# Optimization experiments

Measured on AMD Instinct MI355X. Metric: run time of the kernel, lower is better.

## Reference

```python
import jax, jax.numpy as jnp
import numpy as np

N_GRAPHS = 64
NODES_PER_G = 640
N = N_GRAPHS * NODES_PER_G      # 40960 nodes
DEG = 16
E = N * DEG                     # 655360 edges
D = 128                         # hidden_dim == out_dim
POS = 16                        # pos_enc_dim
L = 4                           # n GatedGCN-LSPE layers
N_ATOM = 28
N_BOND = 4
EPS = 1e-6
BN_EPS = 1e-5


def _lin(x, w, b):
    return x @ w + b


def _bn(x, g, b):
    # torch BatchNorm1d training forward: biased batch stats
    m = x.mean(0)
    v = x.var(0)
    return (x - m) * jax.lax.rsqrt(v + BN_EPS) * g + b


def setup_inputs() -> dict:
    key = jax.random.key(0)
    ks = iter(jax.random.split(key, 64))
    def nrm(shape, s=0.1):
        return jax.random.normal(next(ks), shape, dtype=jnp.float32) * s
    h_atoms = jax.random.randint(next(ks), (N,), 0, N_ATOM)
    e_bonds = jax.random.randint(next(ks), (E,), 0, N_BOND)
    # keep edges within each graph of the batch
    epg = E // N_GRAPHS
    off = (jnp.arange(E) // epg) * NODES_PER_G
    src = jax.random.randint(next(ks), (E,), 0, NODES_PER_G) + off
    dst = jax.random.randint(next(ks), (E,), 0, NODES_PER_G) + off
    node_graph_ids = jnp.arange(N) // NODES_PER_G
    return dict(
        h_atoms=h_atoms, e_bonds=e_bonds, src=src, dst=dst,
        node_graph_ids=node_graph_ids,
        p=nrm((N, POS), 1.0),
        W_emb_h=nrm((N_ATOM, D)), W_emb_p=nrm((POS, D)), b_emb_p=nrm((D,)),
        W_emb_e=nrm((N_BOND, D)),
        A1_w=nrm((L, 2 * D, D)), A1_b=nrm((L, D)),
        A2_w=nrm((L, 2 * D, D)), A2_b=nrm((L, D)),
        B1_w=nrm((L, D, D)), B1_b=nrm((L, D)),
        B2_w=nrm((L, D, D)), B2_b=nrm((L, D)),
        B3_w=nrm((L, D, D)), B3_b=nrm((L, D)),
        C1_w=nrm((L, D, D)), C1_b=nrm((L, D)),
        C2_w=nrm((L, D, D)), C2_b=nrm((L, D)),
        bn_h_g=jnp.ones((L, D)), bn_h_b=jnp.zeros((L, D)),
        bn_e_g=jnp.ones((L, D)), bn_e_b=jnp.zeros((L, D)),
        p_out_w=nrm((D, POS)), p_out_b=nrm((POS,)),
        Whp_w=nrm((D + POS, D)), Whp_b=nrm((D,)),
        mlp_w0=nrm((D, D // 2)), mlp_b0=nrm((D // 2,)),
        mlp_w1=nrm((D // 2, D // 4)), mlp_b1=nrm((D // 4,)),
        mlp_w2=nrm((D // 4, 1)), mlp_b2=nrm((1,)),
    )


def _forward(p, W_emb_h, W_emb_p, b_emb_p, W_emb_e,
             A1_w, A1_b, A2_w, A2_b, B1_w, B1_b, B2_w, B2_b, B3_w, B3_b,
             C1_w, C1_b, C2_w, C2_b, bn_h_g, bn_h_b, bn_e_g, bn_e_b,
             p_out_w, p_out_b, Whp_w, Whp_b,
             mlp_w0, mlp_b0, mlp_w1, mlp_b1, mlp_w2, mlp_b2,
             h_atoms, e_bonds, src, dst, node_graph_ids):
    seg = lambda x, idx, n: jax.ops.segment_sum(x, idx, num_segments=n)
    h = W_emb_h[h_atoms]                      # [N,D] atom embedding
    pc = _lin(p, W_emb_p, b_emb_p)            # [N,D] PE embedding
    ef = W_emb_e[e_bonds]                     # [E,D] bond embedding
    for l in range(L):
        h_in, p_in, e_in = h, pc, ef
        # edge gates: hat_eta_ij = B1 h_i + B2 h_j + B3 e_ij (u=src, v=dst)
        hat_eta = (_lin(h, B1_w[l], B1_b[l])[src]
                   + _lin(h, B2_w[l], B2_b[l])[dst]
                   + _lin(ef, B3_w[l], B3_b[l]))          # [E,D]
        sig = jax.nn.sigmoid(hat_eta)
        eta = sig / (seg(sig, dst, N)[dst] + EPS)          # normalized gate
        hp = jnp.concatenate([h, pc], axis=-1)             # [N,2D]
        h_new = _lin(hp, A1_w[l], A1_b[l]) + seg(eta * _lin(hp, A2_w[l], A2_b[l])[src], dst, N)
        p_new = _lin(pc, C1_w[l], C1_b[l]) + seg(eta * _lin(pc, C2_w[l], C2_b[l])[src], dst, N)
        h_new = jax.nn.relu(_bn(h_new, bn_h_g[l], bn_h_b[l]))
        e_new = jax.nn.relu(_bn(hat_eta, bn_e_g[l], bn_e_b[l]))
        p_new = jnp.tanh(p_new)
        h = h_in + h_new       # residual (in_dim==out_dim)
        pc = p_in + p_new
        ef = e_in + e_new
    # pe_init == 'rand_walk' post-processing
    po = _lin(pc, p_out_w, p_out_b)                        # [N,POS]
    po = po - (seg(po, node_graph_ids, N_GRAPHS) / NODES_PER_G)[node_graph_ids]
    po = po / jnp.sqrt(seg(po * po, node_graph_ids, N_GRAPHS))[node_graph_ids]
    hp2 = _lin(jnp.concatenate([h, po], axis=-1), Whp_w, Whp_b)
    hg = seg(hp2, node_graph_ids, N_GRAPHS) / NODES_PER_G  # mean readout [G,D]
    y = jax.nn.relu(_lin(hg, mlp_w0, mlp_b0))
    y = jax.nn.relu(_lin(y, mlp_w1, mlp_b1))
    return _lin(y, mlp_w2, mlp_b2)                         # [G,1]


def reference(h_atoms, e_bonds, src, dst, node_graph_ids, p,
              W_emb_h, W_emb_p, b_emb_p, W_emb_e,
              A1_w, A1_b, A2_w, A2_b, B1_w, B1_b, B2_w, B2_b, B3_w, B3_b,
              C1_w, C1_b, C2_w, C2_b, bn_h_g, bn_h_b, bn_e_g, bn_e_b,
              p_out_w, p_out_b, Whp_w, Whp_b,
              mlp_w0, mlp_b0, mlp_w1, mlp_b1, mlp_w2, mlp_b2):
    return _forward(p, W_emb_h, W_emb_p, b_emb_p, W_emb_e,
                    A1_w, A1_b, A2_w, A2_b, B1_w, B1_b, B2_w, B2_b, B3_w, B3_b,
                    C1_w, C1_b, C2_w, C2_b, bn_h_g, bn_h_b, bn_e_g, bn_e_b,
                    p_out_w, p_out_b, Whp_w, Whp_b,
                    mlp_w0, mlp_b0, mlp_w1, mlp_b1, mlp_w2, mlp_b2,
                    h_atoms, e_bonds, src, dst, node_graph_ids)
```

## Files before the change

kernel.cpp:

```cpp
#include <hip/hip_runtime.h>
#include <math.h>

#define N_NODES 40960
#define N_EDGES 655360
#define NPG     640
#define NGRAPH  64
#define DH      128
#define NLAYERS 4
#define GATE_EPS 1e-6f
#define BN_EPS   1e-5f

#define POOL_BYTES 560000000ull
__device__ __attribute__((aligned(256))) unsigned char g_pool[POOL_BYTES];

using short8  = __attribute__((ext_vector_type(8))) short;
using float4v = __attribute__((ext_vector_type(4))) float;

static __device__ __forceinline__ float sigmoidf_(float x) {
  return 1.f / (1.f + __expf(-x));
}
static __device__ __forceinline__ unsigned short f2bf(float f) {
  unsigned int u = __float_as_uint(f);
  unsigned int r = 0x7FFFu + ((u >> 16) & 1u);
  return (unsigned short)((u + r) >> 16);
}
static __device__ __forceinline__ float bf2f(unsigned short h) {
  return __uint_as_float(((unsigned int)h) << 16);
}

template <int WITH_STATS>
__global__ __launch_bounds__(256)
void egemm(const unsigned short* __restrict__ ef,
           const unsigned short* __restrict__ Wt,
           const float* __restrict__ bias,
           unsigned short* __restrict__ hat,
           const int* __restrict__ srcp, const int* __restrict__ dstp,
           const float* __restrict__ G1, const float* __restrict__ G2,
           float* __restrict__ stats)
{
  __shared__ __align__(16) unsigned char smem[128 * 136 * 2];
  auto Ws   = reinterpret_cast<unsigned short (*)[136]>(smem);
  auto hatL = reinterpret_cast<float (*)[132]>(smem);

  const int t    = threadIdx.x;
  const int w    = t >> 6;
  const int lane = t & 63;
  const int quad = lane >> 4;
  const int l16  = lane & 15;
  const size_t row0 = (size_t)blockIdx.x * 64;

  const size_t arow = row0 + w * 16 + l16;
  short8 a[4];
#pragma unroll
  for (int ks = 0; ks < 4; ++ks)
    a[ks] = *reinterpret_cast<const short8*>(&ef[arow * 128 + ks * 32 + quad * 8]);

#pragma unroll
  for (int i = 0; i < 8; ++i) {
    int flat = i * 256 + t;
    int n = flat >> 4, g = flat & 15;
    *reinterpret_cast<uint4*>(&Ws[n][g * 8]) =
        *reinterpret_cast<const uint4*>(&Wt[n * 128 + g * 8]);
  }
  __syncthreads();

  float4v acc[8];
#pragma unroll
  for (int j = 0; j < 8; ++j) acc[j] = (float4v){0.f, 0.f, 0.f, 0.f};

#pragma unroll
  for (int ks = 0; ks < 4; ++ks) {
#pragma unroll
    for (int j = 0; j < 8; ++j) {
      short8 b = *reinterpret_cast<const short8*>(&Ws[j * 16 + l16][ks * 32 + quad * 8]);
      acc[j] = __builtin_amdgcn_mfma_f32_16x16x32_bf16(a[ks], b, acc[j], 0, 0, 0);
    }
  }

  __syncthreads();
#pragma unroll
  for (int j = 0; j < 8; ++j)
#pragma unroll
    for (int r = 0; r < 4; ++r)
      hatL[w * 16 + quad * 4 + r][j * 16 + l16] = acc[j][r];
  __syncthreads();

  {
    const int r   = t >> 2;
    const int c0  = (t & 3) * 32;
    const size_t row = row0 + r;
    const int si = srcp[row], di = dstp[row];
    const float* g1p = &G1[(size_t)si * 128 + c0];
    const float* g2p = &G2[(size_t)di * 128 + c0];
    const float* bp  = &bias[c0];
#pragma unroll
    for (int q2 = 0; q2 < 4; ++q2) {
      float4 h0 = *reinterpret_cast<const float4*>(&hatL[r][c0 + q2 * 8]);
      float4 h1 = *reinterpret_cast<const float4*>(&hatL[r][c0 + q2 * 8 + 4]);
      float4 b0 = *reinterpret_cast<const float4*>(&bp[q2 * 8]);
      float4 b1 = *reinterpret_cast<const float4*>(&bp[q2 * 8 + 4]);
      float4 x0 = *reinterpret_cast<const float4*>(&g1p[q2 * 8]);
      float4 x1 = *reinterpret_cast<const float4*>(&g1p[q2 * 8 + 4]);
      float4 y0 = *reinterpret_cast<const float4*>(&g2p[q2 * 8]);
      float4 y1 = *reinterpret_cast<const float4*>(&g2p[q2 * 8 + 4]);
      float v[8] = {h0.x + b0.x + x0.x + y0.x, h0.y + b0.y + x0.y + y0.y,
                    h0.z + b0.z + x0.z + y0.z, h0.w + b0.w + x0.w + y0.w,
                    h1.x + b1.x + x1.x + y1.x, h1.y + b1.y + x1.y + y1.y,
                    h1.z + b1.z + x1.z + y1.z, h1.w + b1.w + x1.w + y1.w};
      unsigned int pk[4];
      float vr[8];
#pragma unroll
      for (int i = 0; i < 4; ++i) {
        unsigned short lo = f2bf(v[2 * i]), hi = f2bf(v[2 * i + 1]);
        pk[i] = (unsigned int)lo | ((unsigned int)hi << 16);
        vr[2 * i] = bf2f(lo); vr[2 * i + 1] = bf2f(hi);
      }
      uint4 st; st.x = pk[0]; st.y = pk[1]; st.z = pk[2]; st.w = pk[3];
      *reinterpret_cast<uint4*>(&hat[row * 128 + c0 + q2 * 8]) = st;
      if (WITH_STATS) {
        float4 w0; w0.x = vr[0]; w0.y = vr[1]; w0.z = vr[2]; w0.w = vr[3];
        float4 w1; w1.x = vr[4]; w1.y = vr[5]; w1.z = vr[6]; w1.w = vr[7];
        *reinterpret_cast<float4*>(&hatL[r][c0 + q2 * 8]) = w0;
        *reinterpret_cast<float4*>(&hatL[r][c0 + q2 * 8 + 4]) = w1;
      }
    }
  }

  if constexpr (WITH_STATS) {
    __syncthreads();
    if (t < 128) {
      float s = 0.f, q = 0.f;
#pragma unroll 8
      for (int r = 0; r < 64; ++r) {
        float v = hatL[r][t];
        s += v; q += v * v;
      }
      atomicAdd(&stats[t], s);
      atomicAdd(&stats[128 + t], q);
    }
  }
}

__global__ __launch_bounds__(256)
void ngemm6(const unsigned short* __restrict__ hp,
            const unsigned short* __restrict__ WtL,
            const float* __restrict__ B1b, const float* __restrict__ B2b,
            const float* __restrict__ A1b, const float* __restrict__ A2b,
            const float* __restrict__ C1b, const float* __restrict__ C2b,
            float* __restrict__ B1h, float* __restrict__ B2h,
            float* __restrict__ A1hp, float* __restrict__ A2hp,
            float* __restrict__ C1p, float* __restrict__ C2p)
{
  __shared__ unsigned short As[64][264];

  const int t    = threadIdx.x;
  const int w    = t >> 6;
  const int lane = t & 63;
  const int quad = lane >> 4;
  const int l16  = lane & 15;
  const size_t row0 = (size_t)blockIdx.x * 64;

#pragma unroll
  for (int i = 0; i < 8; ++i) {
    int flat = i * 256 + t;
    int r = flat >> 5, g = flat & 31;
    *reinterpret_cast<uint4*>(&As[r][g * 8]) =
        *reinterpret_cast<const uint4*>(&hp[(row0 + r) * 256 + g * 8]);
  }
  __syncthreads();

  const unsigned short* Wm[6] = {WtL, WtL + 16384, WtL + 49152, WtL + 81920,
                                 WtL + 114688, WtL + 131072};
  const int Kk[6]   = {128, 128, 256, 256, 128, 128};
  const int koff[6] = {0, 0, 0, 0, 128, 128};
  const float* bs[6] = {B1b, B2b, A1b, A2b, C1b, C2b};
  float* outp[6] = {B1h, B2h, A1hp, A2hp, C1p, C2p};

  for (int m = 0; m < 6; ++m) {
    const unsigned short* W = Wm[m];
    const int K = Kk[m], ko = koff[m];
    float4v acc[8];
#pragma unroll
    for (int j = 0; j < 8; ++j) acc[j] = (float4v){0.f, 0.f, 0.f, 0.f};
    for (int ks = 0; ks < K / 32; ++ks) {
      short8 a = *reinterpret_cast<const short8*>(&As[w * 16 + l16][ko + ks * 32 + quad * 8]);
#pragma unroll
      for (int j = 0; j < 8; ++j) {
        short8 b = *reinterpret_cast<const short8*>(&W[(size_t)(j * 16 + l16) * K + ks * 32 + quad * 8]);
        acc[j] = __builtin_amdgcn_mfma_f32_16x16x32_bf16(a, b, acc[j], 0, 0, 0);
      }
    }
    float* o = outp[m];
    const float* bb = bs[m];
#pragma unroll
    for (int j = 0; j < 8; ++j) {
      int col = j * 16 + l16;
      float bc = bb[col];
#pragma unroll
      for (int r = 0; r < 4; ++r) {
        size_t orow = row0 + w * 16 + quad * 4 + r;
        o[orow * 128 + col] = acc[j][r] + bc;
      }
    }
  }
}

__global__ void prep_weights(const float* __restrict__ B1, const float* __restrict__ B2,
                             const float* __restrict__ B3, const float* __restrict__ A1,
                             const float* __restrict__ A2, const float* __restrict__ C1,
                             const float* __restrict__ C2, unsigned short* __restrict__ Wt)
{
  int idx = blockIdx.x * 256 + threadIdx.x;
  if (idx >= 4 * 147456) return;
  int layer = idx / 147456;
  int o = idx - layer * 147456;
  const float* src; int K, local;
  if (o < 16384)       { src = B1 + layer * 16384; local = o;          K = 128; }
  else if (o < 32768)  { src = B2 + layer * 16384; local = o - 16384;  K = 128; }
  else if (o < 49152)  { src = B3 + layer * 16384; local = o - 32768;  K = 128; }
  else if (o < 81920)  { src = A1 + layer * 32768; local = o - 49152;  K = 256; }
  else if (o < 114688) { src = A2 + layer * 32768; local = o - 81920;  K = 256; }
  else if (o < 131072) { src = C1 + layer * 16384; local = o - 114688; K = 128; }
  else                 { src = C2 + layer * 16384; local = o - 131072; K = 128; }
  int n = local / K, k = local - n * K;
  Wt[idx] = f2bf(src[k * 128 + n]);
}

__global__ void convert_hp(const float* __restrict__ h, const float* __restrict__ pc,
                           unsigned short* __restrict__ hp)
{
  int t = blockIdx.x * 256 + threadIdx.x;
  if (t >= N_NODES * 64) return;
  int n = t >> 6, part = t & 63;
  float4 v = (part < 32) ? reinterpret_cast<const float4*>(h)[n * 32 + part]
                         : reinterpret_cast<const float4*>(pc)[n * 32 + (part - 32)];
  ushort4 o;
  o.x = f2bf(v.x); o.y = f2bf(v.y); o.z = f2bf(v.z); o.w = f2bf(v.w);
  reinterpret_cast<ushort4*>(hp)[n * 64 + part] = o;
}

__global__ void embed_nodes_k(const int* __restrict__ idx, const float* __restrict__ table,
                              float* __restrict__ out, int M)
{
  int t = blockIdx.x * 256 + threadIdx.x;
  if (t < M * 32) {
    int r = t >> 5, c = t & 31;
    reinterpret_cast<float4*>(out)[t] =
        reinterpret_cast<const float4*>(table)[idx[r] * 32 + c];
  }
}

__global__ void embed_edges_bf(const int* __restrict__ bonds, const int* __restrict__ eidx,
                               const float* __restrict__ table,
                               unsigned short* __restrict__ out, int M)
{
  int t = blockIdx.x * 256 + threadIdx.x;
  if (t < M * 32) {
    int r = t >> 5, c = t & 31;
    float4 v = reinterpret_cast<const float4*>(table)[bonds[eidx[r]] * 32 + c];
    ushort4 o;
    o.x = f2bf(v.x); o.y = f2bf(v.y); o.z = f2bf(v.z); o.w = f2bf(v.w);
    reinterpret_cast<ushort4*>(out)[t] = o;
  }
}

__global__ void hist_k(const int* __restrict__ dstI, int* __restrict__ deg, int E)
{
  int e = blockIdx.x * 256 + threadIdx.x;
  if (e < E) atomicAdd(&deg[dstI[e]], 1);
}

__global__ void scan_k(const int* __restrict__ deg, int* __restrict__ row_start,
                       int* __restrict__ cursor, int n)
{
  __shared__ int buf[1024];
  __shared__ int carry;
  int t = threadIdx.x;
  if (t == 0) carry = 0;
  __syncthreads();
  for (int b0 = 0; b0 < n; b0 += 1024) {
    int v = (b0 + t < n) ? deg[b0 + t] : 0;
    buf[t] = v;
    __syncthreads();
    for (int off = 1; off < 1024; off <<= 1) {
      int add = (t >= off) ? buf[t - off] : 0;
      __syncthreads();
      buf[t] += add;
      __syncthreads();
    }
    int incl = buf[t];
    int excl = carry + incl - v;
    if (b0 + t < n) { row_start[b0 + t] = excl; cursor[b0 + t] = excl; }
    __syncthreads();
    if (t == 1023) carry += incl;
    __syncthreads();
  }
  if (t == 0) row_start[n] = carry;
}

__global__ void fill_k(const int* __restrict__ dstI, int* __restrict__ cursor,
                       int* __restrict__ eidx, int E)
{
  int e = blockIdx.x * 256 + threadIdx.x;
  if (e < E) {
    int p = atomicAdd(&cursor[dstI[e]], 1);
    eidx[p] = e;
  }
}

__global__ void permute_sd(const int* __restrict__ eidx, const int* __restrict__ srcI,
                           const int* __restrict__ dstI, int* __restrict__ srcp,
                           int* __restrict__ dstp, int E)
{
  int e = blockIdx.x * 256 + threadIdx.x;
  if (e < E) {
    int o = eidx[e];
    srcp[e] = srcI[o];
    dstp[e] = dstI[o];
  }
}

template <int EF_UPD>
__global__ __launch_bounds__(256)
void gate_agg4(const unsigned short* __restrict__ hat, const int* __restrict__ row_start,
               const int* __restrict__ srcp,
               const float* __restrict__ A1hp, const float* __restrict__ A2hp,
               const float* __restrict__ C1p, const float* __restrict__ C2p,
               float* __restrict__ hraw, float* __restrict__ pc,
               unsigned short* __restrict__ ef, const float* __restrict__ ss_e,
               unsigned short* __restrict__ hp)
{
  int t = threadIdx.x;
  int node = blockIdx.x * 4 + (t >> 6);
  int lane = t & 63;
  int c = lane * 2;
  int beg = row_start[node], end = row_start[node + 1];

  float s0 = 0.f, s1 = 0.f;
  for (int e = beg; e < end; ++e) {
    ushort2 hv = *reinterpret_cast<const ushort2*>(&hat[(size_t)e * 128 + c]);
    s0 += sigmoidf_(bf2f(hv.x));
    s1 += sigmoidf_(bf2f(hv.y));
  }
  float inv0 = 1.f / (s0 + GATE_EPS);
  float inv1 = 1.f / (s1 + GATE_EPS);

  float2 eA, eB;
  if (EF_UPD) {
    eA = *reinterpret_cast<const float2*>(&ss_e[c]);
    eB = *reinterpret_cast<const float2*>(&ss_e[128 + c]);
  }

  float ha0 = 0.f, ha1 = 0.f, pa0 = 0.f, pa1 = 0.f;
  for (int e = beg; e < end; ++e) {
    int s = srcp[e];
    ushort2 hv = *reinterpret_cast<const ushort2*>(&hat[(size_t)e * 128 + c]);
    float hx = bf2f(hv.x), hy = bf2f(hv.y);
    float w0 = sigmoidf_(hx) * inv0;
    float w1 = sigmoidf_(hy) * inv1;
    float2 a2 = *reinterpret_cast<const float2*>(&A2hp[(size_t)s * 128 + c]);
    float2 c2 = *reinterpret_cast<const float2*>(&C2p[(size_t)s * 128 + c]);
    ha0 += w0 * a2.x; ha1 += w1 * a2.y;
    pa0 += w0 * c2.x; pa1 += w1 * c2.y;
    if (EF_UPD) {
      ushort2 ev = *reinterpret_cast<ushort2*>(&ef[(size_t)e * 128 + c]);
      float ex = bf2f(ev.x) + fmaxf(hx * eA.x + eB.x, 0.f);
      float ey = bf2f(ev.y) + fmaxf(hy * eA.y + eB.y, 0.f);
      ushort2 eo; eo.x = f2bf(ex); eo.y = f2bf(ey);
      *reinterpret_cast<ushort2*>(&ef[(size_t)e * 128 + c]) = eo;
    }
  }
  size_t ix = (size_t)node * 128 + c;
  float2 a1 = *reinterpret_cast<const float2*>(&A1hp[ix]);
  float2 c1 = *reinterpret_cast<const float2*>(&C1p[ix]);
  float2 hv; hv.x = a1.x + ha0; hv.y = a1.y + ha1;
  *reinterpret_cast<float2*>(&hraw[ix]) = hv;
  float2 pv = *reinterpret_cast<float2*>(&pc[ix]);
  pv.x += tanhf(c1.x + pa0);
  pv.y += tanhf(c1.y + pa1);
  *reinterpret_cast<float2*>(&pc[ix]) = pv;
  ushort2 ph; ph.x = f2bf(pv.x); ph.y = f2bf(pv.y);
  *reinterpret_cast<ushort2*>(&hp[(size_t)node * 256 + 128 + c]) = ph;
}

__global__ __launch_bounds__(128)
void col_stats(const float* __restrict__ x, float* __restrict__ stats, int rowsPerBlock)
{
  int d = threadIdx.x;
  size_t r0 = (size_t)blockIdx.x * rowsPerBlock;
  float s = 0.f, q = 0.f;
  for (int i = 0; i < rowsPerBlock; ++i) {
    float v = x[(r0 + i) * 128 + d];
    s += v; q += v * v;
  }
  atomicAdd(&stats[d], s);
  atomicAdd(&stats[128 + d], q);
}

__global__ void bn_finalize(const float* __restrict__ stats, const float* __restrict__ g,
                            const float* __restrict__ b, float invM, float* __restrict__ ss)
{
  int c = threadIdx.x;
  float m = stats[c] * invM;
  float v = stats[128 + c] * invM - m * m;
  float A = rsqrtf(v + BN_EPS) * g[c];
  ss[c] = A;
  ss[128 + c] = b[c] - m * A;
}

__global__ void apply_h(float* __restrict__ dest, const float* __restrict__ xraw,
                        const float* __restrict__ ss, unsigned short* __restrict__ hp,
                        int total4)
{
  int t = blockIdx.x * 256 + threadIdx.x;
  if (t >= total4) return;
  int c4 = t & 31, n = t >> 5;
  float4 x = reinterpret_cast<const float4*>(xraw)[t];
  float4 A = reinterpret_cast<const float4*>(ss)[c4];
  float4 B = reinterpret_cast<const float4*>(ss + 128)[c4];
  float4 dv = reinterpret_cast<float4*>(dest)[t];
  dv.x += fmaxf(x.x * A.x + B.x, 0.f);
  dv.y += fmaxf(x.y * A.y + B.y, 0.f);
  dv.z += fmaxf(x.z * A.z + B.z, 0.f);
  dv.w += fmaxf(x.w * A.w + B.w, 0.f);
  reinterpret_cast<float4*>(dest)[t] = dv;
  ushort4 o;
  o.x = f2bf(dv.x); o.y = f2bf(dv.y); o.z = f2bf(dv.z); o.w = f2bf(dv.w);
  *reinterpret_cast<ushort4*>(&hp[(size_t)n * 256 + c4 * 4]) = o;
}

template <int MODE>
__global__ __launch_bounds__(256)
void gemm_k(const float* __restrict__ Xa, int Ka,
            const float* __restrict__ Xb, int Kb,
            const float* __restrict__ W,
            const float* __restrict__ bias,
            float* __restrict__ out,
            float* __restrict__ hg, float inv_nodes, int npg)
{
  __shared__ float Xs[16][68];
  __shared__ float Ws[16][128];
  __shared__ float red[8][128];

  const int t  = threadIdx.x;
  const int ty = t >> 5;
  const int tx = t & 31;
  const int row0 = blockIdx.x * 64;
  const int K = Ka + Kb;

  float acc[8][4];
#pragma unroll
  for (int i = 0; i < 8; ++i)
#pragma unroll
    for (int j = 0; j < 4; ++j) acc[i][j] = 0.f;

  const int xr = t >> 2;
  const int xk = (t & 3) << 2;
  const int wr = t >> 5;
  const int wc = tx << 2;

  for (int kk = 0; kk < K; kk += 16) {
    const float* xbase; int ldk, kloc;
    if (kk < Ka) { xbase = Xa; ldk = Ka; kloc = kk; }
    else         { xbase = Xb; ldk = Kb; kloc = kk - Ka; }
    float4 xv = *reinterpret_cast<const float4*>(
        &xbase[(size_t)(row0 + xr) * ldk + kloc + xk]);
    Xs[xk + 0][xr] = xv.x; Xs[xk + 1][xr] = xv.y;
    Xs[xk + 2][xr] = xv.z; Xs[xk + 3][xr] = xv.w;

    float4 wv0 = *reinterpret_cast<const float4*>(&W[(size_t)(kk + wr) * 128 + wc]);
    float4 wv1 = *reinterpret_cast<const float4*>(&W[(size_t)(kk + wr + 8) * 128 + wc]);
    *reinterpret_cast<float4*>(&Ws[wr][wc])     = wv0;
    *reinterpret_cast<float4*>(&Ws[wr + 8][wc]) = wv1;
    __syncthreads();

#pragma unroll
    for (int k = 0; k < 16; ++k) {
      float4 b4 = *reinterpret_cast<const float4*>(&Ws[k][wc]);
      float4 a0 = *reinterpret_cast<const float4*>(&Xs[k][ty << 3]);
      float4 a1 = *reinterpret_cast<const float4*>(&Xs[k][(ty << 3) + 4]);
      float a[8] = {a0.x, a0.y, a0.z, a0.w, a1.x, a1.y, a1.z, a1.w};
      float b[4] = {b4.x, b4.y, b4.z, b4.w};
#pragma unroll
      for (int i = 0; i < 8; ++i) {
        acc[i][0] += a[i] * b[0];
        acc[i][1] += a[i] * b[1];
        acc[i][2] += a[i] * b[2];
        acc[i][3] += a[i] * b[3];
      }
    }
    __syncthreads();
  }

  float4 bb = *reinterpret_cast<const float4*>(&bias[wc]);
  float bv[4] = {bb.x, bb.y, bb.z, bb.w};

  if (MODE == 0) {
#pragma unroll
    for (int i = 0; i < 8; ++i) {
      int r = row0 + (ty << 3) + i;
      float4 ov;
      ov.x = acc[i][0] + bv[0]; ov.y = acc[i][1] + bv[1];
      ov.z = acc[i][2] + bv[2]; ov.w = acc[i][3] + bv[3];
      *reinterpret_cast<float4*>(&out[(size_t)r * 128 + wc]) = ov;
    }
  } else {
    float csum[4] = {0, 0, 0, 0};
#pragma unroll
    for (int i = 0; i < 8; ++i) {
      csum[0] += acc[i][0]; csum[1] += acc[i][1];
      csum[2] += acc[i][2]; csum[3] += acc[i][3];
    }
#pragma unroll
    for (int j = 0; j < 4; ++j) red[ty][wc + j] = csum[j];
    __syncthreads();
    if (ty == 0) {
      int g = row0 / npg;
#pragma unroll
      for (int j = 0; j < 4; ++j) {
        float s = 0;
#pragma unroll
        for (int q = 0; q < 8; ++q) s += red[q][wc + j];
        atomicAdd(&hg[(size_t)g * 128 + wc + j], (s + 64.f * bv[j]) * inv_nodes);
      }
    }
  }
}

__global__ __launch_bounds__(256)
void po_gemm(const float* __restrict__ pc, const float* __restrict__ w,
             const float* __restrict__ b, float* __restrict__ po)
{
  __shared__ float pcs[16][128];
  __shared__ float wl[128][16];
  int t = threadIdx.x;
  int n0 = blockIdx.x * 16;
  for (int i = t; i < 512; i += 256) {
    int r = i >> 5, c = (i & 31) << 2;
    *reinterpret_cast<float4*>(&pcs[r][c]) =
        *reinterpret_cast<const float4*>(&pc[(size_t)(n0 + r) * 128 + c]);
  }
  for (int i = t; i < 512; i += 256) {
    int r = i >> 2, c = (i & 3) << 2;
    *reinterpret_cast<float4*>(&wl[r][c]) =
        *reinterpret_cast<const float4*>(&w[r * 16 + c]);
  }
  __syncthreads();
  int i = t >> 4, j = t & 15;
  float acc = b[j];
  for (int k = 0; k < 128; ++k) acc += pcs[i][k] * wl[k][j];
  po[(size_t)(n0 + i) * 16 + j] = acc;
}

__global__ __launch_bounds__(256)
void pe_norm(float* __restrict__ po)
{
  int g = blockIdx.x;
  int t = threadIdx.x;
  int j = t & 15, grp = t >> 4;
  __shared__ float red[16][16];
  __shared__ float mean_s[16];
  __shared__ float nrm_s[16];
  size_t bse = (size_t)g * NPG * 16;
  float s = 0.f;
  for (int i = grp; i < NPG; i += 16) s += po[bse + i * 16 + j];
  red[grp][j] = s;
  __syncthreads();
  if (grp == 0) {
    float m = 0.f;
    for (int q = 0; q < 16; ++q) m += red[q][j];
    mean_s[j] = m / NPG;
  }
  __syncthreads();
  float m = mean_s[j];
  float q2 = 0.f;
  for (int i = grp; i < NPG; i += 16) {
    float c = po[bse + i * 16 + j] - m;
    q2 += c * c;
  }
  red[grp][j] = q2;
  __syncthreads();
  if (grp == 0) {
    float v = 0.f;
    for (int q = 0; q < 16; ++q) v += red[q][j];
    nrm_s[j] = sqrtf(v);
  }
  __syncthreads();
  float inv = 1.f / nrm_s[j];
  for (int i = grp; i < NPG; i += 16) {
    size_t ix = bse + i * 16 + j;
    po[ix] = (po[ix] - m) * inv;
  }
}

__global__ __launch_bounds__(256)
void mlp_head(const float* __restrict__ hg,
              const float* __restrict__ w0, const float* __restrict__ b0,
              const float* __restrict__ w1, const float* __restrict__ b1,
              const float* __restrict__ w2, const float* __restrict__ b2,
              float* __restrict__ out)
{
  __shared__ float hs[64 * 128];
  __shared__ float y0[64 * 64];
  __shared__ float y1[64 * 32];
  int t = threadIdx.x;
  for (int i = t; i < 64 * 128 / 4; i += 256)
    reinterpret_cast<float4*>(hs)[i] = reinterpret_cast<const float4*>(hg)[i];
  __syncthreads();
  for (int o = t; o < 64 * 64; o += 256) {
    int i = o >> 6, j = o & 63;
    float a = b0[j];
    for (int k = 0; k < 128; ++k) a += hs[i * 128 + k] * w0[k * 64 + j];
    y0[o] = fmaxf(a, 0.f);
  }
  __syncthreads();
  for (int o = t; o < 64 * 32; o += 256) {
    int i = o >> 5, j = o & 31;
    float a = b1[j];
    for (int k = 0; k < 64; ++k) a += y0[i * 64 + k] * w1[k * 32 + j];
    y1[o] = fmaxf(a, 0.f);
  }
  __syncthreads();
  if (t < 64) {
    float a = b2[0];
    for (int k = 0; k < 32; ++k) a += y1[t * 32 + k] * w2[k];
    out[t] = a;
  }
}

__global__ void fill_sentinel(float* out, int n, float v)
{
  int t = blockIdx.x * 256 + threadIdx.x;
  if (t < n) out[t] = v;
}

extern "C" void kernel_launch(void* const* d_in, const int* in_sizes, int n_in,
                              void* d_out, int out_size, void* d_ws, size_t ws_size,
                              hipStream_t stream)
{
  const int*   h_atoms = (const int*)d_in[0];
  const int*   e_bonds = (const int*)d_in[1];
  const int*   srcI    = (const int*)d_in[2];
  const int*   dstI    = (const int*)d_in[3];
  const float* p_in    = (const float*)d_in[5];
  const float* W_emb_h = (const float*)d_in[6];
  const float* W_emb_p = (const float*)d_in[7];
  const float* b_emb_p = (const float*)d_in[8];
  const float* W_emb_e = (const float*)d_in[9];
  const float* A1_w = (const float*)d_in[10];
  const float* A1_b = (const float*)d_in[11];
  const float* A2_w = (const float*)d_in[12];
  const float* A2_b = (const float*)d_in[13];
  const float* B1_w = (const float*)d_in[14];
  const float* B1_b = (const float*)d_in[15];
  const float* B2_w = (const float*)d_in[16];
  const float* B2_b = (const float*)d_in[17];
  const float* B3_w = (const float*)d_in[18];
  const float* B3_b = (const float*)d_in[19];
  const float* C1_w = (const float*)d_in[20];
  const float* C1_b = (const float*)d_in[21];
  const float* C2_w = (const float*)d_in[22];
  const float* C2_b = (const float*)d_in[23];
  const float* bn_h_g = (const float*)d_in[24];
  const float* bn_h_b = (const float*)d_in[25];
  const float* bn_e_g = (const float*)d_in[26];
  const float* bn_e_b = (const float*)d_in[27];
  const float* p_out_w = (const float*)d_in[28];
  const float* p_out_b = (const float*)d_in[29];
  const float* Whp_w   = (const float*)d_in[30];
  const float* Whp_b   = (const float*)d_in[31];
  const float* mlp_w0  = (const float*)d_in[32];
  const float* mlp_b0  = (const float*)d_in[33];
  const float* mlp_w1  = (const float*)d_in[34];
  const float* mlp_b1  = (const float*)d_in[35];
  const float* mlp_w2  = (const float*)d_in[36];
  const float* mlp_b2  = (const float*)d_in[37];

  static void* pool_ptr = nullptr;
  if (!pool_ptr) {
    if (hipGetSymbolAddress(&pool_ptr, HIP_SYMBOL(g_pool)) != hipSuccess || !pool_ptr) {
      fill_sentinel<<<dim3(1), dim3(256), 0, stream>>>((float*)d_out, out_size, 12345.0f);
      return;
    }
  }

  float* fbase = (float*)pool_ptr;
  size_t fo = 0;
  auto carvef = [&](size_t nf) { float* r = fbase + fo; fo += nf; return r; };
  float* h    = carvef((size_t)N_NODES * DH);
  float* pc   = carvef((size_t)N_NODES * DH);
  float* B1h  = carvef((size_t)N_NODES * DH);
  float* B2h  = carvef((size_t)N_NODES * DH);
  float* A1hp = carvef((size_t)N_NODES * DH);
  float* A2hp = carvef((size_t)N_NODES * DH);
  float* C1p  = carvef((size_t)N_NODES * DH);
  float* C2p  = carvef((size_t)N_NODES * DH);
  float* po   = carvef((size_t)N_NODES * 16);
  float* hg   = carvef(NGRAPH * 128);
  float* estats = carvef(256);
  float* hstats = carvef(256);
  float* ss_e   = carvef(256);
  float* ss_h   = carvef(256);
  float* hraw = B1h;

  unsigned short* ubase = (unsigned short*)(fbase + fo);
  unsigned short* ef_bf  = ubase;
  unsigned short* hat_bf = ef_bf + (size_t)N_EDGES * DH;
  unsigned short* hp_bf  = hat_bf + (size_t)N_EDGES * DH;
  unsigned short* Wt_bf  = hp_bf + (size_t)N_NODES * 256;
  int* ibase = (int*)(Wt_bf + 4 * 147456);
  int* deg       = ibase;
  int* row_start = deg + N_NODES;
  int* cursor    = row_start + (N_NODES + 3);
  int* eidx      = cursor + N_NODES;
  int* srcp      = eidx + N_EDGES;
  int* dstp      = srcp + N_EDGES;

  dim3 b256(256);

  prep_weights<<<dim3((4 * 147456 + 255) / 256), b256, 0, stream>>>(
      B1_w, B2_w, B3_w, A1_w, A2_w, C1_w, C2_w, Wt_bf);

  hipMemsetAsync(deg, 0, N_NODES * sizeof(int), stream);
  hist_k<<<dim3((N_EDGES + 255) / 256), b256, 0, stream>>>(dstI, deg, N_EDGES);
  scan_k<<<dim3(1), dim3(1024), 0, stream>>>(deg, row_start, cursor, N_NODES);
  fill_k<<<dim3((N_EDGES + 255) / 256), b256, 0, stream>>>(dstI, cursor, eidx, N_EDGES);
  permute_sd<<<dim3((N_EDGES + 255) / 256), b256, 0, stream>>>(eidx, srcI, dstI, srcp, dstp, N_EDGES);

  embed_nodes_k<<<dim3((N_NODES * 32 + 255) / 256), b256, 0, stream>>>(h_atoms, W_emb_h, h, N_NODES);
  embed_edges_bf<<<dim3((N_EDGES * 32 + 255) / 256), b256, 0, stream>>>(
      e_bonds, eidx, W_emb_e, ef_bf, N_EDGES);
  gemm_k<0><<<dim3(N_NODES / 64), b256, 0, stream>>>(
      p_in, 16, nullptr, 0, W_emb_p, b_emb_p, pc, nullptr, 0.f, NPG);
  convert_hp<<<dim3(N_NODES * 64 / 256), b256, 0, stream>>>(h, pc, hp_bf);

  const dim3 gNode64(N_NODES / 64), gEdge(N_EDGES / 64);

  for (int l = 0; l < NLAYERS; ++l) {
    const unsigned short* WtL = Wt_bf + (size_t)l * 147456;
    const unsigned short* WtB3 = WtL + 32768;
    const bool last = (l == NLAYERS - 1);

    ngemm6<<<gNode64, b256, 0, stream>>>(hp_bf, WtL,
        B1_b + l * 128, B2_b + l * 128, A1_b + l * 128, A2_b + l * 128,
        C1_b + l * 128, C2_b + l * 128, B1h, B2h, A1hp, A2hp, C1p, C2p);

    if (!last) {
      hipMemsetAsync(estats, 0, 256 * sizeof(float), stream);
      egemm<1><<<gEdge, b256, 0, stream>>>(ef_bf, WtB3, B3_b + l * 128, hat_bf,
          srcp, dstp, B1h, B2h, estats);
      bn_finalize<<<dim3(1), dim3(128), 0, stream>>>(
          estats, bn_e_g + l * 128, bn_e_b + l * 128, 1.f / N_EDGES, ss_e);
      gate_agg4<1><<<dim3(N_NODES / 4), b256, 0, stream>>>(
          hat_bf, row_start, srcp, A1hp, A2hp, C1p, C2p, hraw, pc, ef_bf, ss_e, hp_bf);
    } else {
      egemm<0><<<gEdge, b256, 0, stream>>>(ef_bf, WtB3, B3_b + l * 128, hat_bf,
          srcp, dstp, B1h, B2h, nullptr);
      gate_agg4<0><<<dim3(N_NODES / 4), b256, 0, stream>>>(
          hat_bf, row_start, srcp, A1hp, A2hp, C1p, C2p, hraw, pc, nullptr, nullptr, hp_bf);
    }

    hipMemsetAsync(hstats, 0, 256 * sizeof(float), stream);
    col_stats<<<dim3(128), dim3(128), 0, stream>>>(hraw, hstats, N_NODES / 128);
    bn_finalize<<<dim3(1), dim3(128), 0, stream>>>(
        hstats, bn_h_g + l * 128, bn_h_b + l * 128, 1.f / N_NODES, ss_h);

    apply_h<<<dim3(N_NODES * 32 / 256), b256, 0, stream>>>(
        h, hraw, ss_h, hp_bf, N_NODES * 32);
  }

  po_gemm<<<dim3(N_NODES / 16), b256, 0, stream>>>(pc, p_out_w, p_out_b, po);
  pe_norm<<<dim3(NGRAPH), b256, 0, stream>>>(po);

  hipMemsetAsync(hg, 0, NGRAPH * 128 * sizeof(float), stream);
  gemm_k<2><<<dim3(N_NODES / 64), b256, 0, stream>>>(
      h, 128, po, 16, Whp_w, Whp_b, nullptr, hg, 1.f / NPG, NPG);

  mlp_head<<<dim3(1), b256, 0, stream>>>(
      hg, mlp_w0, mlp_b0, mlp_w1, mlp_b1, mlp_w2, mlp_b2, (float*)d_out);
}
```

Measured before the change: 3.381 ms.

## Fuse sigmoid gate-sum into edge GEMM, use bf16 B1h/B2h, multi-tile edge blocks

The edge GEMM kernel now computes sigmoid of each hat value and accumulates per-destination sums with segmented atomics into a new ssum buffer. The aggregation kernel reads that sum instead of making its own pass over the hat edges. B1h/B2h are stored as bf16 to halve gather traffic, and each edge block processes 4 tiles so the weight load and the stats atomics are amortised. The cost is an extra memset of a full node×128 float buffer each layer, a large number of atomics, and lower precision for the gathered node terms.

```diff
diff --git a/kernel.cpp b/kernel.cpp
--- a/kernel.cpp
+++ b/kernel.cpp
@@ -9,8 +9,9 @@
 #define NLAYERS 4
 #define GATE_EPS 1e-6f
 #define BN_EPS   1e-5f
-
-#define POOL_BYTES 560000000ull
+#define ETPB    4
+
+#define POOL_BYTES 580000000ull
 __device__ __attribute__((aligned(256))) unsigned char g_pool[POOL_BYTES];
 
 using short8  = __attribute__((ext_vector_type(8))) short;
@@ -35,12 +36,145 @@
            const float* __restrict__ bias,
            unsigned short* __restrict__ hat,
            const int* __restrict__ srcp, const int* __restrict__ dstp,
-           const float* __restrict__ G1, const float* __restrict__ G2,
-           float* __restrict__ stats)
-{
-  __shared__ __align__(16) unsigned char smem[128 * 136 * 2];
-  auto Ws   = reinterpret_cast<unsigned short (*)[136]>(smem);
-  auto hatL = reinterpret_cast<float (*)[132]>(smem);
+           const unsigned short* __restrict__ G1, const unsigned short* __restrict__ G2,
+           float* __restrict__ stats, float* __restrict__ ssum)
+{
+  __shared__ unsigned short Ws[128][136];
+  __shared__ float hatL[64][132];
+  __shared__ int dstL[64];
+
+  const int t    = threadIdx.x;
+  const int w    = t >> 6;
+  const int lane = t & 63;
+  const int quad = lane >> 4;
+  const int l16  = lane & 15;
+
+#pragma unroll
+  for (int i = 0; i < 8; ++i) {
+    int flat = i * 256 + t;
+    int n = flat >> 4, g = flat & 15;
+    *reinterpret_cast<uint4*>(&Ws[n][g * 8]) =
+        *reinterpret_cast<const uint4*>(&Wt[n * 128 + g * 8]);
+  }
+  __syncthreads();
+
+  float stat_s = 0.f, stat_q = 0.f;
+
+  for (int tile = 0; tile < ETPB; ++tile) {
+    const size_t row0 = ((size_t)blockIdx.x * ETPB + tile) * 64;
+
+    const size_t arow = row0 + w * 16 + l16;
+    short8 a[4];
+#pragma unroll
+    for (int ks = 0; ks < 4; ++ks)
+      a[ks] = *reinterpret_cast<const short8*>(&ef[arow * 128 + ks * 32 + quad * 8]);
+
+    float4v acc[8];
+#pragma unroll
+    for (int j = 0; j < 8; ++j) acc[j] = (float4v){0.f, 0.f, 0.f, 0.f};
+#pragma unroll
+    for (int ks = 0; ks < 4; ++ks)
+#pragma unroll
+      for (int j = 0; j < 8; ++j) {
+        short8 b = *reinterpret_cast<const short8*>(&Ws[j * 16 + l16][ks * 32 + quad * 8]);
+        acc[j] = __builtin_amdgcn_mfma_f32_16x16x32_bf16(a[ks], b, acc[j], 0, 0, 0);
+      }
+
+    if (tile) __syncthreads();
+#pragma unroll
+    for (int j = 0; j < 8; ++j)
+#pragma unroll
+      for (int r = 0; r < 4; ++r)
+        hatL[w * 16 + quad * 4 + r][j * 16 + l16] = acc[j][r];
+    __syncthreads();
+
+    {
+      const int r = t >> 2, seg = t & 3;
+      const size_t row = row0 + r;
+      const int si = srcp[row], di = dstp[row];
+      if (seg == 0) dstL[r] = di;
+      const unsigned short* g1p = &G1[(size_t)si * 128];
+      const unsigned short* g2p = &G2[(size_t)di * 128];
+#pragma unroll
+      for (int q2 = 0; q2 < 4; ++q2) {
+        const int cc = seg * 32 + (((q2 + seg) & 3) << 3);
+        float4 h0 = *reinterpret_cast<const float4*>(&hatL[r][cc]);
+        float4 h1 = *reinterpret_cast<const float4*>(&hatL[r][cc + 4]);
+        float4 b0 = *reinterpret_cast<const float4*>(&bias[cc]);
+        float4 b1 = *reinterpret_cast<const float4*>(&bias[cc + 4]);
+        uint4 g1 = *reinterpret_cast<const uint4*>(&g1p[cc]);
+        uint4 g2 = *reinterpret_cast<const uint4*>(&g2p[cc]);
+        float hv[8] = {h0.x, h0.y, h0.z, h0.w, h1.x, h1.y, h1.z, h1.w};
+        float bv[8] = {b0.x, b0.y, b0.z, b0.w, b1.x, b1.y, b1.z, b1.w};
+        unsigned int g1w[4] = {g1.x, g1.y, g1.z, g1.w};
+        unsigned int g2w[4] = {g2.x, g2.y, g2.z, g2.w};
+        unsigned int pk[4];
+        float vr[8];
+#pragma unroll
+        for (int i = 0; i < 4; ++i) {
+          float vlo = hv[2 * i]     + bv[2 * i]
+                    + bf2f((unsigned short)(g1w[i] & 0xffffu))
+                    + bf2f((unsigned short)(g2w[i] & 0xffffu));
+          float vhi = hv[2 * i + 1] + bv[2 * i + 1]
+                    + bf2f((unsigned short)(g1w[i] >> 16))
+                    + bf2f((unsigned short)(g2w[i] >> 16));
+          unsigned short lo = f2bf(vlo), hi = f2bf(vhi);
+          pk[i] = (unsigned int)lo | ((unsigned int)hi << 16);
+          vr[2 * i] = bf2f(lo); vr[2 * i + 1] = bf2f(hi);
+        }
+        uint4 st; st.x = pk[0]; st.y = pk[1]; st.z = pk[2]; st.w = pk[3];
+        *reinterpret_cast<uint4*>(&hat[row * 128 + cc]) = st;
+        float4 w0; w0.x = vr[0]; w0.y = vr[1]; w0.z = vr[2]; w0.w = vr[3];
+        float4 w1; w1.x = vr[4]; w1.y = vr[5]; w1.z = vr[6]; w1.w = vr[7];
+        *reinterpret_cast<float4*>(&hatL[r][cc])     = w0;
+        *reinterpret_cast<float4*>(&hatL[r][cc + 4]) = w1;
+      }
+    }
+    __syncthreads();
+
+    if (WITH_STATS && t < 128) {
+      float s = 0.f, q = 0.f;
+#pragma unroll 8
+      for (int r = 0; r < 64; ++r) {
+        float v = hatL[r][t];
+        s += v; q += v * v;
+      }
+      stat_s += s; stat_q += q;
+    }
+    if (t >= 128) {
+      const int c = t - 128;
+      float run = 0.f;
+      int prev = dstL[0];
+      for (int r = 0; r < 64; ++r) {
+        int d = dstL[r];
+        float sg = sigmoidf_(hatL[r][c]);
+        if (d != prev) {
+          atomicAdd(&ssum[(size_t)prev * 128 + c], run);
+          run = 0.f; prev = d;
+        }
+        run += sg;
+      }
+      atomicAdd(&ssum[(size_t)prev * 128 + c], run);
+    }
+  }
+
+  if (WITH_STATS && t < 128) {
+    atomicAdd(&stats[t], stat_s);
+    atomicAdd(&stats[128 + t], stat_q);
+  }
+}
+
+__global__ __launch_bounds__(256)
+void ngemm6(const unsigned short* __restrict__ hp,
+            const unsigned short* __restrict__ WtL,
+            const float* __restrict__ B1b, const float* __restrict__ B2b,
+            const float* __restrict__ A1b, const float* __restrict__ A2b,
+            const float* __restrict__ C1b, const float* __restrict__ C2b,
+            unsigned short* __restrict__ B1h, unsigned short* __restrict__ B2h,
+            float* __restrict__ A1hp, float* __restrict__ A2hp,
+            float* __restrict__ C1p, float* __restrict__ C2p)
+{
+  __shared__ unsigned short As[64][264];
 
   const int t    = threadIdx.x;
   const int w    = t >> 6;
@@ -49,117 +183,6 @@
   const int l16  = lane & 15;
   const size_t row0 = (size_t)blockIdx.x * 64;
 
-  const size_t arow = row0 + w * 16 + l16;
-  short8 a[4];
-#pragma unroll
-  for (int ks = 0; ks < 4; ++ks)
-    a[ks] = *reinterpret_cast<const short8*>(&ef[arow * 128 + ks * 32 + quad * 8]);
-
-#pragma unroll
-  for (int i = 0; i < 8; ++i) {
-    int flat = i * 256 + t;
-    int n = flat >> 4, g = flat & 15;
-    *reinterpret_cast<uint4*>(&Ws[n][g * 8]) =
-        *reinterpret_cast<const uint4*>(&Wt[n * 128 + g * 8]);
-  }
-  __syncthreads();
-
-  float4v acc[8];
-#pragma unroll
-  for (int j = 0; j < 8; ++j) acc[j] = (float4v){0.f, 0.f, 0.f, 0.f};
-
-#pragma unroll
-  for (int ks = 0; ks < 4; ++ks) {
-#pragma unroll
-    for (int j = 0; j < 8; ++j) {
-      short8 b = *reinterpret_cast<const short8*>(&Ws[j * 16 + l16][ks * 32 + quad * 8]);
-      acc[j] = __builtin_amdgcn_mfma_f32_16x16x32_bf16(a[ks], b, acc[j], 0, 0, 0);
-    }
-  }
-
-  __syncthreads();
-#pragma unroll
-  for (int j = 0; j < 8; ++j)
-#pragma unroll
-    for (int r = 0; r < 4; ++r)
-      hatL[w * 16 + quad * 4 + r][j * 16 + l16] = acc[j][r];
-  __syncthreads();
-
-  {
-    const int r   = t >> 2;
-    const int c0  = (t & 3) * 32;
-    const size_t row = row0 + r;
-    const int si = srcp[row], di = dstp[row];
-    const float* g1p = &G1[(size_t)si * 128 + c0];
-    const float* g2p = &G2[(size_t)di * 128 + c0];
-    const float* bp  = &bias[c0];
-#pragma unroll
-    for (int q2 = 0; q2 < 4; ++q2) {
-      float4 h0 = *reinterpret_cast<const float4*>(&hatL[r][c0 + q2 * 8]);
-      float4 h1 = *reinterpret_cast<const float4*>(&hatL[r][c0 + q2 * 8 + 4]);
-      float4 b0 = *reinterpret_cast<const float4*>(&bp[q2 * 8]);
-      float4 b1 = *reinterpret_cast<const float4*>(&bp[q2 * 8 + 4]);
-      float4 x0 = *reinterpret_cast<const float4*>(&g1p[q2 * 8]);
-      float4 x1 = *reinterpret_cast<const float4*>(&g1p[q2 * 8 + 4]);
-      float4 y0 = *reinterpret_cast<const float4*>(&g2p[q2 * 8]);
-      float4 y1 = *reinterpret_cast<const float4*>(&g2p[q2 * 8 + 4]);
-      float v[8] = {h0.x + b0.x + x0.x + y0.x, h0.y + b0.y + x0.y + y0.y,
-                    h0.z + b0.z + x0.z + y0.z, h0.w + b0.w + x0.w + y0.w,
-                    h1.x + b1.x + x1.x + y1.x, h1.y + b1.y + x1.y + y1.y,
-                    h1.z + b1.z + x1.z + y1.z, h1.w + b1.w + x1.w + y1.w};
-      unsigned int pk[4];
-      float vr[8];
-#pragma unroll
-      for (int i = 0; i < 4; ++i) {
-        unsigned short lo = f2bf(v[2 * i]), hi = f2bf(v[2 * i + 1]);
-        pk[i] = (unsigned int)lo | ((unsigned int)hi << 16);
-        vr[2 * i] = bf2f(lo); vr[2 * i + 1] = bf2f(hi);
-      }
-      uint4 st; st.x = pk[0]; st.y = pk[1]; st.z = pk[2]; st.w = pk[3];
-      *reinterpret_cast<uint4*>(&hat[row * 128 + c0 + q2 * 8]) = st;
-      if (WITH_STATS) {
-        float4 w0; w0.x = vr[0]; w0.y = vr[1]; w0.z = vr[2]; w0.w = vr[3];
-        float4 w1; w1.x = vr[4]; w1.y = vr[5]; w1.z = vr[6]; w1.w = vr[7];
-        *reinterpret_cast<float4*>(&hatL[r][c0 + q2 * 8]) = w0;
-        *reinterpret_cast<float4*>(&hatL[r][c0 + q2 * 8 + 4]) = w1;
-      }
-    }
-  }
-
-  if constexpr (WITH_STATS) {
-    __syncthreads();
-    if (t < 128) {
-      float s = 0.f, q = 0.f;
-#pragma unroll 8
-      for (int r = 0; r < 64; ++r) {
-        float v = hatL[r][t];
-        s += v; q += v * v;
-      }
-      atomicAdd(&stats[t], s);
-      atomicAdd(&stats[128 + t], q);
-    }
-  }
-}
-
-__global__ __launch_bounds__(256)
-void ngemm6(const unsigned short* __restrict__ hp,
-            const unsigned short* __restrict__ WtL,
-            const float* __restrict__ B1b, const float* __restrict__ B2b,
-            const float* __restrict__ A1b, const float* __restrict__ A2b,
-            const float* __restrict__ C1b, const float* __restrict__ C2b,
-            float* __restrict__ B1h, float* __restrict__ B2h,
-            float* __restrict__ A1hp, float* __restrict__ A2hp,
-            float* __restrict__ C1p, float* __restrict__ C2p)
-{
-  __shared__ unsigned short As[64][264];
-
-  const int t    = threadIdx.x;
-  const int w    = t >> 6;
-  const int lane = t & 63;
-  const int quad = lane >> 4;
-  const int l16  = lane & 15;
-  const size_t row0 = (size_t)blockIdx.x * 64;
-
 #pragma unroll
   for (int i = 0; i < 8; ++i) {
     int flat = i * 256 + t;
@@ -174,7 +197,8 @@
   const int Kk[6]   = {128, 128, 256, 256, 128, 128};
   const int koff[6] = {0, 0, 0, 0, 128, 128};
   const float* bs[6] = {B1b, B2b, A1b, A2b, C1b, C2b};
-  float* outp[6] = {B1h, B2h, A1hp, A2hp, C1p, C2p};
+  float* outf[6] = {nullptr, nullptr, A1hp, A2hp, C1p, C2p};
+  unsigned short* outb[2] = {B1h, B2h};
 
   for (int m = 0; m < 6; ++m) {
     const unsigned short* W = Wm[m];
@@ -190,16 +214,30 @@
         acc[j] = __builtin_amdgcn_mfma_f32_16x16x32_bf16(a, b, acc[j], 0, 0, 0);
       }
     }
-    float* o = outp[m];
     const float* bb = bs[m];
-#pragma unroll
-    for (int j = 0; j < 8; ++j) {
-      int col = j * 16 + l16;
-      float bc = bb[col];
-#pragma unroll
-      for (int r = 0; r < 4; ++r) {
-        size_t orow = row0 + w * 16 + quad * 4 + r;
-        o[orow * 128 + col] = acc[j][r] + bc;
+    if (m < 2) {
+      unsigned short* o = outb[m];
+#pragma unroll
+      for (int j = 0; j < 8; ++j) {
+        int col = j * 16 + l16;
+        float bc = bb[col];
+#pragma unroll
+        for (int r = 0; r < 4; ++r) {
+          size_t orow = row0 + w * 16 + quad * 4 + r;
+          o[orow * 128 + col] = f2bf(acc[j][r] + bc);
+        }
+      }
+    } else {
+      float* o = outf[m];
+#pragma unroll
+      for (int j = 0; j < 8; ++j) {
+        int col = j * 16 + l16;
+        float bc = bb[col];
+#pragma unroll
+        for (int r = 0; r < 4; ++r) {
+          size_t orow = row0 + w * 16 + quad * 4 + r;
+          o[orow * 128 + col] = acc[j][r] + bc;
+        }
       }
     }
   }
@@ -322,8 +360,8 @@
 
 template <int EF_UPD>
 __global__ __launch_bounds__(256)
-void gate_agg4(const unsigned short* __restrict__ hat, const int* __restrict__ row_start,
-               const int* __restrict__ srcp,
+void gate_agg5(const unsigned short* __restrict__ hat, const int* __restrict__ row_start,
+               const int* __restrict__ srcp, const float* __restrict__ ssum,
                const float* __restrict__ A1hp, const float* __restrict__ A2hp,
                const float* __restrict__ C1p, const float* __restrict__ C2p,
                float* __restrict__ hraw, float* __restrict__ pc,
@@ -336,14 +374,9 @@
   int c = lane * 2;
   int beg = row_start[node], end = row_start[node + 1];
 
-  float s0 = 0.f, s1 = 0.f;
-  for (int e = beg; e < end; ++e) {
-    ushort2 hv = *reinterpret_cast<const ushort2*>(&hat[(size_t)e * 128 + c]);
-    s0 += sigmoidf_(bf2f(hv.x));
-    s1 += sigmoidf_(bf2f(hv.y));
-  }
-  float inv0 = 1.f / (s0 + GATE_EPS);
-  float inv1 = 1.f / (s1 + GATE_EPS);
+  float2 sv = *reinterpret_cast<const float2*>(&ssum[(size_t)node * 128 + c]);
+  float inv0 = 1.f / (sv.x + GATE_EPS);
+  float inv1 = 1.f / (sv.y + GATE_EPS);
 
   float2 eA, eB;
   if (EF_UPD) {
@@ -689,25 +722,26 @@
   auto carvef = [&](size_t nf) { float* r = fbase + fo; fo += nf; return r; };
   float* h    = carvef((size_t)N_NODES * DH);
   float* pc   = carvef((size_t)N_NODES * DH);
-  float* B1h  = carvef((size_t)N_NODES * DH);
-  float* B2h  = carvef((size_t)N_NODES * DH);
   float* A1hp = carvef((size_t)N_NODES * DH);
   float* A2hp = carvef((size_t)N_NODES * DH);
   float* C1p  = carvef((size_t)N_NODES * DH);
   float* C2p  = carvef((size_t)N_NODES * DH);
+  float* hraw = carvef((size_t)N_NODES * DH);
+  float* ssum = carvef((size_t)N_NODES * DH);
   float* po   = carvef((size_t)N_NODES * 16);
   float* hg   = carvef(NGRAPH * 128);
   float* estats = carvef(256);
   float* hstats = carvef(256);
   float* ss_e   = carvef(256);
   float* ss_h   = carvef(256);
-  float* hraw = B1h;
 
   unsigned short* ubase = (unsigned short*)(fbase + fo);
   unsigned short* ef_bf  = ubase;
   unsigned short* hat_bf = ef_bf + (size_t)N_EDGES * DH;
   unsigned short* hp_bf  = hat_bf + (size_t)N_EDGES * DH;
-  unsigned short* Wt_bf  = hp_bf + (size_t)N_NODES * 256;
+  unsigned short* b1_bf  = hp_bf + (size_t)N_NODES * 256;
+  unsigned short* b2_bf  = b1_bf + (size_t)N_NODES * DH;
+  unsigned short* Wt_bf  = b2_bf + (size_t)N_NODES * DH;
   int* ibase = (int*)(Wt_bf + 4 * 147456);
   int* deg       = ibase;
   int* row_start = deg + N_NODES;
@@ -734,7 +768,7 @@
       p_in, 16, nullptr, 0, W_emb_p, b_emb_p, pc, nullptr, 0.f, NPG);
   convert_hp<<<dim3(N_NODES * 64 / 256), b256, 0, stream>>>(h, pc, hp_bf);
 
-  const dim3 gNode64(N_NODES / 64), gEdge(N_EDGES / 64);
+  const dim3 gNode64(N_NODES / 64), gEdge(N_EDGES / (64 * ETPB));
 
   for (int l = 0; l < NLAYERS; ++l) {
     const unsigned short* WtL = Wt_bf + (size_t)l * 147456;
@@ -743,21 +777,24 @@
 
     ngemm6<<<gNode64, b256, 0, stream>>>(hp_bf, WtL,
         B1_b + l * 128, B2_b + l * 128, A1_b + l * 128, A2_b + l * 128,
-        C1_b + l * 128, C2_b + l * 128, B1h, B2h, A1hp, A2hp, C1p, C2p);
-
+        C1_b + l * 128, C2_b + l * 128, b1_bf, b2_bf, A1hp, A2hp, C1p, C2p);
+
+    hipMemsetAsync(ssum, 0, (size_t)N_NODES * DH * sizeof(float), stream);
     if (!last) {
       hipMemsetAsync(estats, 0, 256 * sizeof(float), stream);
       egemm<1><<<gEdge, b256, 0, stream>>>(ef_bf, WtB3, B3_b + l * 128, hat_bf,
-          srcp, dstp, B1h, B2h, estats);
+          srcp, dstp, b1_bf, b2_bf, estats, ssum);
       bn_finalize<<<dim3(1), dim3(128), 0, stream>>>(
           estats, bn_e_g + l * 128, bn_e_b + l * 128, 1.f / N_EDGES, ss_e);
-      gate_agg4<1><<<dim3(N_NODES / 4), b256, 0, stream>>>(
-          hat_bf, row_start, srcp, A1hp, A2hp, C1p, C2p, hraw, pc, ef_bf, ss_e, hp_bf);
+      gate_agg5<1><<<dim3(N_NODES / 4), b256, 0, stream>>>(
+          hat_bf, row_start, srcp, ssum, A1hp, A2hp, C1p, C2p, hraw, pc,
+          ef_bf, ss_e, hp_bf);
     } else {
       egemm<0><<<gEdge, b256, 0, stream>>>(ef_bf, WtB3, B3_b + l * 128, hat_bf,
-          srcp, dstp, B1h, B2h, nullptr);
-      gate_agg4<0><<<dim3(N_NODES / 4), b256, 0, stream>>>(
-          hat_bf, row_start, srcp, A1hp, A2hp, C1p, C2p, hraw, pc, nullptr, nullptr, hp_bf);
+          srcp, dstp, b1_bf, b2_bf, nullptr, ssum);
+      gate_agg5<0><<<dim3(N_NODES / 4), b256, 0, stream>>>(
+          hat_bf, row_start, srcp, ssum, A1hp, A2hp, C1p, C2p, hraw, pc,
+          nullptr, nullptr, hp_bf);
     }
 
     hipMemsetAsync(hstats, 0, 256 * sizeof(float), stream);
```

Result: faster. 3.068 ms (-9.2%).
